# Kernel optimization log

Hardware: AMD Instinct MI355X
Metric: run time of the kernel (lower is better)

The kernel has to match this reference:

```python
import jax, jax.numpy as jnp
import numpy as np

B, T, C_IN, HID, WIN = 16384, 20, 256, 256, 3


def tb_mask(T=20, win=3):
    # Faithful replica of TemporalCrossAttent.TB (including its quirky indexing).
    m = np.zeros((T, T), dtype=np.float32)
    for i in range(T):
        if i - win < 0:
            m[i, :win] = 1
        elif i + win >= T:
            m[i, T - win:] = 1
        else:
            m[i - win // 2, i - win // 2:i + win // 2] = 1
    return jnp.asarray(np.where(m == 1, 0.0, -1e22).astype(np.float32))


def setup_inputs() -> dict:
    key = jax.random.key(0)
    k1, k2, k3, k4, k5 = jax.random.split(key, 5)
    scale = 0.05  # xavier-ish init scale for 256x256
    return {
        "feat1": jax.random.normal(k1, (B, T, C_IN), dtype=jnp.float32),
        "feat2": jax.random.normal(k2, (B, T, C_IN), dtype=jnp.float32),
        "Wq": jax.random.normal(k3, (HID, C_IN), dtype=jnp.float32) * scale,
        "Wk": jax.random.normal(k4, (HID, C_IN), dtype=jnp.float32) * scale,
        "Wv": jax.random.normal(k5, (HID, C_IN), dtype=jnp.float32) * scale,
    }


def reference(feat1, feat2, Wq, Wk, Wv):
    # Conv1d(kernel_size=1, bias=False) == pointwise linear over channels.
    mask = tb_mask(T, WIN)  # [T, T] static banded additive mask
    q = jnp.einsum('btc,hc->bth', feat1, Wq)  # [B,T,HID]
    k = jnp.einsum('btc,hc->bth', feat2, Wk)
    v = jnp.einsum('btc,hc->bth', feat2, Wv)
    sim = jnp.einsum('bth,bsh->bts', q, k) / jnp.sqrt(jnp.float32(HID))
    attn = jax.nn.softmax(sim + mask, axis=-1)  # [B,T,T]
    # dropout layers act as identity in eval mode
    return jnp.einsum('bts,bsh->bth', attn, v)  # [B,T,HID]
```

## Files before the change

### kernel.cpp

```cpp
#include <hip/hip_runtime.h>
#include <stdint.h>

#define NBATCH 16384
#define TT     20
#define CC     256
#define FP     260
#define FB     520
#define LDK    264
#define TP     40
#define NT     256

typedef __bf16 bf16x8 __attribute__((ext_vector_type(8)));
typedef float  f32x4  __attribute__((ext_vector_type(4)));

#define GLL16(g, l) __builtin_amdgcn_global_load_lds( \
    (const __attribute__((address_space(1))) uint32_t*)(g), \
    (__attribute__((address_space(3))) uint32_t*)(l), 16, 0, 0)

#define BAR_VM()   do { asm volatile("s_waitcnt vmcnt(0) lgkmcnt(0)" ::: "memory"); \
                        __builtin_amdgcn_s_barrier(); } while (0)
#define BAR_LGKM() do { asm volatile("s_waitcnt lgkmcnt(0)" ::: "memory"); \
                        __builtin_amdgcn_s_barrier(); } while (0)

__constant__ int8_t c_CNT[TT] = {3,3,4,2,2,2,2,2,2,2,2,2,2,2,2,2,0,3,3,3};
__constant__ int8_t c_OFF[TT] = {0,3,6,10,12,14,16,18,20,22,24,26,28,30,32,34,0,36,39,42};
__constant__ int8_t c_PT[45]  = {0,0,0,1,1,1,2,2,2,2,3,3,4,4,5,5,6,6,7,7,8,8,9,9,
                                 10,10,11,11,12,12,13,13,14,14,15,15,17,17,17,18,18,18,19,19,19};
__constant__ int8_t c_PS[45]  = {0,1,2,0,1,2,0,1,2,3,3,4,4,5,5,6,6,7,7,8,8,9,9,10,
                                 10,11,11,12,12,13,13,14,14,15,15,16,17,18,19,17,18,19,17,18,19};

__device__ __forceinline__ uint16_t f2bf(float f) {
    __bf16 b = (__bf16)f;
    return __builtin_bit_cast(uint16_t, b);
}
__device__ __forceinline__ uint32_t pk2(float a, float b) {
    return (uint32_t)f2bf(a) | ((uint32_t)f2bf(b) << 16);
}
__device__ __forceinline__ float bflo(uint32_t u) { return __builtin_bit_cast(float, u << 16); }
__device__ __forceinline__ float bfhi(uint32_t u) { return __builtin_bit_cast(float, u & 0xffff0000u); }

__global__ void prep1_kernel(const float* __restrict__ Wq, const float* __restrict__ Wk,
                             const float* __restrict__ Wv, uint16_t* __restrict__ mqkT,
                             uint16_t* __restrict__ wvb) {
    const int n = blockIdx.x;
    const int k = threadIdx.x;
    float acc = 0.f;
    for (int h = 0; h < CC; ++h)
        acc = fmaf(Wk[h * CC + n], Wq[h * CC + k], acc);
    mqkT[n * CC + k] = f2bf(acc * 0.0625f);
    wvb[n * CC + k]  = f2bf(Wv[n * CC + k]);
}

__global__ void prep2_kernel(const uint16_t* __restrict__ mqkT, const uint16_t* __restrict__ wvb,
                             uint16_t* __restrict__ BqS, uint16_t* __restrict__ BvS) {
    const int bid = blockIdx.x;
    const int m  = bid >> 5;
    const int w  = (bid >> 3) & 3;
    const int kk = bid & 7;
    const int ct   = threadIdx.x >> 6;
    const int lane = threadIdx.x & 63;
    const uint16_t* src = m ? wvb : mqkT;
    uint16_t*       dst = m ? BvS : BqS;
    const int n   = w * 64 + ct * 16 + (lane & 15);
    const int col = kk * 32 + ((lane >> 4) << 3);
    uint4 v = *(const uint4*)(src + n * CC + col);
    *(uint4*)(dst + ((size_t)((w * 32 + kk * 4 + ct) * 64 + lane) << 3)) = v;
}

__device__ __forceinline__ bf16x8 ldb(const uint16_t* __restrict__ s, int r, int u) {
    return __builtin_bit_cast(bf16x8, *(const uint4*)(s + r * FB + (u << 3)));
}

__global__ __launch_bounds__(NT, 3)
void attn_main(const float* __restrict__ f1g, const float* __restrict__ f2g,
               const uint16_t* __restrict__ BqS, const uint16_t* __restrict__ BvS,
               float* __restrict__ outg) {
    __shared__ char smem[53632];
    float*    sF1f  = (float*)smem;
    float*    sF2f  = (float*)(smem + 20800);
    uint16_t* attnL = (uint16_t*)(smem + 41600);
    float*    s_simE = (float*)(smem + 42880);
    uint16_t* sT    = (uint16_t*)(smem + 43072);
    uint16_t* sFb1 = (uint16_t*)sF1f;
    uint16_t* sFb2 = (uint16_t*)sF2f;
    uint16_t* sVT  = (uint16_t*)smem;

    const int tid  = threadIdx.x;
    const int lane = tid & 63;
    const int w    = tid >> 6;
    const int l15  = lane & 15;
    const int q    = lane >> 4;
    const size_t base = (size_t)blockIdx.x * TT * CC;
    const float* f1 = f1g + base;
    const float* f2 = f2g + base;

#pragma unroll
    for (int j = 0; j < 5; ++j) {
        int r = w * 5 + j;
        GLL16(f1 + r * 256 + (lane << 2), sF1f + r * FP);
        GLL16(f2 + r * 256 + (lane << 2), sF2f + r * FP);
    }
    {
        uint32_t* aL = (uint32_t*)attnL;
#pragma unroll
        for (int rep = 0; rep < 2; ++rep) {
            int s = tid + (rep << 8);
            if (s < 320)
                aL[s] = ((s >> 4) == 16 && (s & 15) < 10) ? 0x3F803F80u : 0u;
        }
    }
    BAR_VM();

#pragma unroll
    for (int j = 0; j < 5; ++j) {
        int r = w * 5 + j;
        float4 v1 = *(const float4*)(sF1f + r * FP + (lane << 2));
        float4 v2 = *(const float4*)(sF2f + r * FP + (lane << 2));
        uint2 u1; u1.x = pk2(v1.x, v1.y); u1.y = pk2(v1.z, v1.w);
        uint2 u2; u2.x = pk2(v2.x, v2.y); u2.y = pk2(v2.z, v2.w);
        *(uint2*)(sFb1 + r * FB + (lane << 2)) = u1;
        *(uint2*)(sFb2 + r * FB + (lane << 2)) = u2;
    }
    BAR_LGKM();

    const uint16_t* bq = BqS + ((size_t)w << 14);
    const uint16_t* bv = BvS + ((size_t)w << 14);
    const int rB0 = l15;
    const int rB1 = (16 + l15 < TT) ? 16 + l15 : TT - 1;

    {
        f32x4 acc[4][2];
#pragma unroll
        for (int mt = 0; mt < 4; ++mt)
#pragma unroll
            for (int ct = 0; ct < 2; ++ct)
                acc[mt][ct] = f32x4{0.f, 0.f, 0.f, 0.f};
        __builtin_amdgcn_s_setprio(1);
#pragma unroll
        for (int kk = 0; kk < 8; ++kk) {
            const int u = (kk << 2) + q;
            bf16x8 b0 = ldb(sFb1, rB0, u);
            bf16x8 b1 = ldb(sFb1, rB1, u);
#pragma unroll
            for (int mt = 0; mt < 4; ++mt) {
                bf16x8 am = __builtin_bit_cast(bf16x8,
                    *(const uint4*)(bq + (((kk << 2) + mt) * 64 + lane) * 8));
                acc[mt][0] = __builtin_amdgcn_mfma_f32_16x16x32_bf16(am, b0, acc[mt][0], 0, 0, 0);
                acc[mt][1] = __builtin_amdgcn_mfma_f32_16x16x32_bf16(am, b1, acc[mt][1], 0, 0, 0);
            }
        }
        __builtin_amdgcn_s_setprio(0);
#pragma unroll
        for (int mt = 0; mt < 4; ++mt)
#pragma unroll
            for (int ct = 0; ct < 2; ++ct) {
                int t = ct * 16 + l15;
                if (t < TT) {
                    int h0 = (w << 6) + mt * 16 + (q << 2);
                    uint2 u2;
                    u2.x = pk2(acc[mt][ct][0], acc[mt][ct][1]);
                    u2.y = pk2(acc[mt][ct][2], acc[mt][ct][3]);
                    *(uint2*)&sT[t * LDK + h0] = u2;
                }
            }
    }
    BAR_LGKM();

    if (tid < 180) {
        int d = tid >> 2;
        int p = tid & 3;
        int t = c_PT[d], s = c_PS[d];
        const uint16_t* ap = sT + t * LDK + (p << 3);
        const uint16_t* bp = sFb2 + s * FB + (p << 3);
        float da = 0.f;
#pragma unroll
        for (int c = 0; c < 256; c += 32) {
            uint4 ua = *(const uint4*)(ap + c);
            uint4 ub = *(const uint4*)(bp + c);
            da = fmaf(bflo(ua.x), bflo(ub.x), da);
            da = fmaf(bfhi(ua.x), bfhi(ub.x), da);
            da = fmaf(bflo(ua.y), bflo(ub.y), da);
            da = fmaf(bfhi(ua.y), bfhi(ub.y), da);
            da = fmaf(bflo(ua.z), bflo(ub.z), da);
            da = fmaf(bfhi(ua.z), bfhi(ub.z), da);
            da = fmaf(bflo(ua.w), bflo(ub.w), da);
            da = fmaf(bfhi(ua.w), bfhi(ub.w), da);
        }
        da += __shfl_xor(da, 1);
        da += __shfl_xor(da, 2);
        if (p == 0) {
            float e = __expf(da);
            attnL[t * 32 + s] = f2bf(e);
            s_simE[d] = e;
        }
    }
    {
        f32x4 av[2][4];
#pragma unroll
        for (int rt = 0; rt < 2; ++rt)
#pragma unroll
            for (int ct = 0; ct < 4; ++ct)
                av[rt][ct] = f32x4{0.f, 0.f, 0.f, 0.f};
        __builtin_amdgcn_s_setprio(1);
#pragma unroll
        for (int kk = 0; kk < 8; ++kk) {
            const int u = (kk << 2) + q;
            bf16x8 a0 = ldb(sFb2, rB0, u);
            bf16x8 a1 = ldb(sFb2, rB1, u);
#pragma unroll
            for (int ct = 0; ct < 4; ++ct) {
                bf16x8 bm = __builtin_bit_cast(bf16x8,
                    *(const uint4*)(bv + (((kk << 2) + ct) * 64 + lane) * 8));
                av[0][ct] = __builtin_amdgcn_mfma_f32_16x16x32_bf16(a0, bm, av[0][ct], 0, 0, 0);
                av[1][ct] = __builtin_amdgcn_mfma_f32_16x16x32_bf16(a1, bm, av[1][ct], 0, 0, 0);
            }
        }
        __builtin_amdgcn_s_setprio(0);
#pragma unroll
        for (int ct = 0; ct < 4; ++ct) {
            int h = (w << 6) + ct * 16 + l15;
            {
                uint2 u2;
                u2.x = pk2(av[0][ct][0], av[0][ct][1]);
                u2.y = pk2(av[0][ct][2], av[0][ct][3]);
                *(uint2*)&sVT[h * TP + (q << 2)] = u2;
            }
            {
                uint2 u2;
                if (q == 0) {
                    u2.x = pk2(av[1][ct][0], av[1][ct][1]);
                    u2.y = pk2(av[1][ct][2], av[1][ct][3]);
                } else { u2.x = 0u; u2.y = 0u; }
                *(uint2*)&sVT[h * TP + 16 + (q << 2)] = u2;
            }
        }
    }
    BAR_LGKM();

    {
        bf16x8 pa0 = __builtin_bit_cast(bf16x8, *(const uint4*)&attnL[l15 * 32 + (q << 3)]);
        bf16x8 pa1 = __builtin_bit_cast(bf16x8, *(const uint4*)&attnL[(16 + l15) * 32 + (q << 3)]);
        const f32x4 z = f32x4{0.f, 0.f, 0.f, 0.f};
        f32x4 o[2][4];
        __builtin_amdgcn_s_setprio(1);
#pragma unroll
        for (int ct = 0; ct < 4; ++ct) {
            bf16x8 pb = __builtin_bit_cast(bf16x8,
                *(const uint4*)&sVT[((w << 6) + ct * 16 + l15) * TP + (q << 3)]);
            o[0][ct] = __builtin_amdgcn_mfma_f32_16x16x32_bf16(pa0, pb, z, 0, 0, 0);
            o[1][ct] = __builtin_amdgcn_mfma_f32_16x16x32_bf16(pa1, pb, z, 0, 0, 0);
        }
        __builtin_amdgcn_s_setprio(0);
#pragma unroll
        for (int rt = 0; rt < 2; ++rt)
#pragma unroll
            for (int j = 0; j < 4; ++j) {
                int t = rt * 16 + (q << 2) + j;
                if (t < TT) {
                    int cnt = c_CNT[t], off = c_OFF[t];
                    float rs = (cnt == 0) ? 20.0f : s_simE[off];
#pragma unroll
                    for (int jj = 1; jj < 4; ++jj)
                        if (jj < cnt) rs += s_simE[off + jj];
                    float iv = __builtin_amdgcn_rcpf(rs);
                    float* op = outg + base + (size_t)t * CC + (w << 6) + l15;
#pragma unroll
                    for (int ct = 0; ct < 4; ++ct)
                        op[ct * 16] = o[rt][ct][j] * iv;
                }
            }
    }
}

extern "C" void kernel_launch(void* const* d_in, const int* in_sizes, int n_in,
                              void* d_out, int out_size, void* d_ws, size_t ws_size,
                              hipStream_t stream) {
    const float* feat1 = (const float*)d_in[0];
    const float* feat2 = (const float*)d_in[1];
    const float* Wq    = (const float*)d_in[2];
    const float* Wk    = (const float*)d_in[3];
    const float* Wv    = (const float*)d_in[4];
    uint16_t* mqkT = (uint16_t*)d_ws;
    uint16_t* wvb  = mqkT + CC * CC;
    uint16_t* BqS  = wvb  + CC * CC;
    uint16_t* BvS  = BqS  + CC * CC;

    prep1_kernel<<<CC, CC, 0, stream>>>(Wq, Wk, Wv, mqkT, wvb);
    prep2_kernel<<<64, NT, 0, stream>>>(mqkT, wvb, BqS, BvS);
    attn_main<<<NBATCH, NT, 0, stream>>>(feat1, feat2, BqS, BvS, (float*)d_out);
}
```

Measured before the change: 384.1 us.

## Make attention blocks persistent over 32 batches with register-prefetched double-buffered inputs

Each workgroup now handles 32 batch elements in a loop instead of one. While it computes the current element, it loads the next element's feat1/feat2 into registers and converts them to bf16 into an alternate LDS buffer, replacing the global_load_lds path with fp32 staging. This is meant to hide global load latency and amortize launch and setup overhead. In exchange, the grid shrinks to 512 blocks (a few per CU), register pressure rises, and launch bounds drop to 2 waves-per-EU occupancy, which may reduce latency hiding.

```diff
diff --git a/kernel.cpp b/kernel.cpp
--- a/kernel.cpp
+++ b/kernel.cpp
@@ -4,21 +4,14 @@
 #define NBATCH 16384
 #define TT     20
 #define CC     256
-#define FP     260
-#define FB     520
-#define LDK    264
-#define TP     40
+#define LDB    264
+#define TP     32
 #define NT     256
+#define BPB    32
 
 typedef __bf16 bf16x8 __attribute__((ext_vector_type(8)));
 typedef float  f32x4  __attribute__((ext_vector_type(4)));
 
-#define GLL16(g, l) __builtin_amdgcn_global_load_lds( \
-    (const __attribute__((address_space(1))) uint32_t*)(g), \
-    (__attribute__((address_space(3))) uint32_t*)(l), 16, 0, 0)
-
-#define BAR_VM()   do { asm volatile("s_waitcnt vmcnt(0) lgkmcnt(0)" ::: "memory"); \
-                        __builtin_amdgcn_s_barrier(); } while (0)
 #define BAR_LGKM() do { asm volatile("s_waitcnt lgkmcnt(0)" ::: "memory"); \
                         __builtin_amdgcn_s_barrier(); } while (0)
 
@@ -68,60 +61,24 @@
 }
 
 __device__ __forceinline__ bf16x8 ldb(const uint16_t* __restrict__ s, int r, int u) {
-    return __builtin_bit_cast(bf16x8, *(const uint4*)(s + r * FB + (u << 3)));
-}
-
-__global__ __launch_bounds__(NT, 3)
+    return __builtin_bit_cast(bf16x8, *(const uint4*)(s + r * LDB + (u << 3)));
+}
+
+__global__ __launch_bounds__(NT, 2)
 void attn_main(const float* __restrict__ f1g, const float* __restrict__ f2g,
                const uint16_t* __restrict__ BqS, const uint16_t* __restrict__ BvS,
                float* __restrict__ outg) {
-    __shared__ char smem[53632];
-    float*    sF1f  = (float*)smem;
-    float*    sF2f  = (float*)(smem + 20800);
-    uint16_t* attnL = (uint16_t*)(smem + 41600);
-    float*    s_simE = (float*)(smem + 42880);
-    uint16_t* sT    = (uint16_t*)(smem + 43072);
-    uint16_t* sFb1 = (uint16_t*)sF1f;
-    uint16_t* sFb2 = (uint16_t*)sF2f;
-    uint16_t* sVT  = (uint16_t*)smem;
+    __shared__ uint16_t smem[30048];
+    uint16_t* sVT    = smem + 21120;
+    uint16_t* attnL  = smem + 29312;
+    float*    s_simE = (float*)(smem + 29952);
 
     const int tid  = threadIdx.x;
     const int lane = tid & 63;
     const int w    = tid >> 6;
     const int l15  = lane & 15;
     const int q    = lane >> 4;
-    const size_t base = (size_t)blockIdx.x * TT * CC;
-    const float* f1 = f1g + base;
-    const float* f2 = f2g + base;
-
-#pragma unroll
-    for (int j = 0; j < 5; ++j) {
-        int r = w * 5 + j;
-        GLL16(f1 + r * 256 + (lane << 2), sF1f + r * FP);
-        GLL16(f2 + r * 256 + (lane << 2), sF2f + r * FP);
-    }
-    {
-        uint32_t* aL = (uint32_t*)attnL;
-#pragma unroll
-        for (int rep = 0; rep < 2; ++rep) {
-            int s = tid + (rep << 8);
-            if (s < 320)
-                aL[s] = ((s >> 4) == 16 && (s & 15) < 10) ? 0x3F803F80u : 0u;
-        }
-    }
-    BAR_VM();
-
-#pragma unroll
-    for (int j = 0; j < 5; ++j) {
-        int r = w * 5 + j;
-        float4 v1 = *(const float4*)(sF1f + r * FP + (lane << 2));
-        float4 v2 = *(const float4*)(sF2f + r * FP + (lane << 2));
-        uint2 u1; u1.x = pk2(v1.x, v1.y); u1.y = pk2(v1.z, v1.w);
-        uint2 u2; u2.x = pk2(v2.x, v2.y); u2.y = pk2(v2.z, v2.w);
-        *(uint2*)(sFb1 + r * FB + (lane << 2)) = u1;
-        *(uint2*)(sFb2 + r * FB + (lane << 2)) = u2;
-    }
-    BAR_LGKM();
+    const size_t bbase = (size_t)blockIdx.x * BPB * TT * CC;
 
     const uint16_t* bq = BqS + ((size_t)w << 14);
     const uint16_t* bv = BvS + ((size_t)w << 14);
@@ -129,146 +86,209 @@
     const int rB1 = (16 + l15 < TT) ? 16 + l15 : TT - 1;
 
     {
-        f32x4 acc[4][2];
-#pragma unroll
-        for (int mt = 0; mt < 4; ++mt)
-#pragma unroll
-            for (int ct = 0; ct < 2; ++ct)
-                acc[mt][ct] = f32x4{0.f, 0.f, 0.f, 0.f};
-        __builtin_amdgcn_s_setprio(1);
-#pragma unroll
-        for (int kk = 0; kk < 8; ++kk) {
-            const int u = (kk << 2) + q;
-            bf16x8 b0 = ldb(sFb1, rB0, u);
-            bf16x8 b1 = ldb(sFb1, rB1, u);
-#pragma unroll
-            for (int mt = 0; mt < 4; ++mt) {
-                bf16x8 am = __builtin_bit_cast(bf16x8,
-                    *(const uint4*)(bq + (((kk << 2) + mt) * 64 + lane) * 8));
-                acc[mt][0] = __builtin_amdgcn_mfma_f32_16x16x32_bf16(am, b0, acc[mt][0], 0, 0, 0);
-                acc[mt][1] = __builtin_amdgcn_mfma_f32_16x16x32_bf16(am, b1, acc[mt][1], 0, 0, 0);
-            }
-        }
-        __builtin_amdgcn_s_setprio(0);
-#pragma unroll
-        for (int mt = 0; mt < 4; ++mt)
-#pragma unroll
-            for (int ct = 0; ct < 2; ++ct) {
-                int t = ct * 16 + l15;
-                if (t < TT) {
-                    int h0 = (w << 6) + mt * 16 + (q << 2);
-                    uint2 u2;
-                    u2.x = pk2(acc[mt][ct][0], acc[mt][ct][1]);
-                    u2.y = pk2(acc[mt][ct][2], acc[mt][ct][3]);
-                    *(uint2*)&sT[t * LDK + h0] = u2;
-                }
-            }
+        const float* f1 = f1g + bbase;
+        const float* f2 = f2g + bbase;
+        float4 va[5], vb[5];
+#pragma unroll
+        for (int j = 0; j < 5; ++j) {
+            int s = tid + (j << 8);
+            va[j] = *(const float4*)(f1 + (s << 2));
+            vb[j] = *(const float4*)(f2 + (s << 2));
+        }
+        {
+            uint32_t* aL = (uint32_t*)attnL;
+#pragma unroll
+            for (int rep = 0; rep < 2; ++rep) {
+                int s = tid + (rep << 8);
+                if (s < 320)
+                    aL[s] = ((s >> 4) == 16 && (s & 15) < 10) ? 0x3F803F80u : 0u;
+            }
+        }
+#pragma unroll
+        for (int j = 0; j < 5; ++j) {
+            int s  = tid + (j << 8);
+            int r  = s >> 6;
+            int c4 = (s & 63) << 2;
+            uint2 u1; u1.x = pk2(va[j].x, va[j].y); u1.y = pk2(va[j].z, va[j].w);
+            uint2 u2; u2.x = pk2(vb[j].x, vb[j].y); u2.y = pk2(vb[j].z, vb[j].w);
+            *(uint2*)&smem[r * LDB + c4] = u1;
+            *(uint2*)&smem[5280 + r * LDB + c4] = u2;
+        }
     }
     BAR_LGKM();
 
-    if (tid < 180) {
-        int d = tid >> 2;
-        int p = tid & 3;
-        int t = c_PT[d], s = c_PS[d];
-        const uint16_t* ap = sT + t * LDK + (p << 3);
-        const uint16_t* bp = sFb2 + s * FB + (p << 3);
-        float da = 0.f;
-#pragma unroll
-        for (int c = 0; c < 256; c += 32) {
-            uint4 ua = *(const uint4*)(ap + c);
-            uint4 ub = *(const uint4*)(bp + c);
-            da = fmaf(bflo(ua.x), bflo(ub.x), da);
-            da = fmaf(bfhi(ua.x), bfhi(ub.x), da);
-            da = fmaf(bflo(ua.y), bflo(ub.y), da);
-            da = fmaf(bfhi(ua.y), bfhi(ub.y), da);
-            da = fmaf(bflo(ua.z), bflo(ub.z), da);
-            da = fmaf(bfhi(ua.z), bfhi(ub.z), da);
-            da = fmaf(bflo(ua.w), bflo(ub.w), da);
-            da = fmaf(bfhi(ua.w), bfhi(ub.w), da);
-        }
-        da += __shfl_xor(da, 1);
-        da += __shfl_xor(da, 2);
-        if (p == 0) {
-            float e = __expf(da);
-            attnL[t * 32 + s] = f2bf(e);
-            s_simE[d] = e;
-        }
-    }
-    {
-        f32x4 av[2][4];
-#pragma unroll
-        for (int rt = 0; rt < 2; ++rt)
-#pragma unroll
-            for (int ct = 0; ct < 4; ++ct)
-                av[rt][ct] = f32x4{0.f, 0.f, 0.f, 0.f};
-        __builtin_amdgcn_s_setprio(1);
-#pragma unroll
-        for (int kk = 0; kk < 8; ++kk) {
-            const int u = (kk << 2) + q;
-            bf16x8 a0 = ldb(sFb2, rB0, u);
-            bf16x8 a1 = ldb(sFb2, rB1, u);
+    for (int i = 0; i < BPB; ++i) {
+        const int curOf = (i & 1) ? 10560 : 0;
+        const int nxtOf = (i & 1) ? 0 : 10560;
+        const bool hasNext = (i + 1 < BPB);
+        const uint16_t* f1b = smem + curOf;
+        const uint16_t* f2b = smem + curOf + 5280;
+        uint16_t* sT = smem + nxtOf;
+        uint16_t* w2 = smem + nxtOf + 5280;
+
+        float4 pa[5], pb[5];
+        if (hasNext) {
+            const float* f1n = f1g + bbase + (size_t)(i + 1) * TT * CC;
+            const float* f2n = f2g + bbase + (size_t)(i + 1) * TT * CC;
+#pragma unroll
+            for (int j = 0; j < 5; ++j) {
+                int s = tid + (j << 8);
+                pa[j] = *(const float4*)(f1n + (s << 2));
+                pb[j] = *(const float4*)(f2n + (s << 2));
+            }
+            __builtin_amdgcn_sched_barrier(0);
+        }
+
+        {
+            f32x4 acc[4][2];
+#pragma unroll
+            for (int mt = 0; mt < 4; ++mt)
+#pragma unroll
+                for (int ct = 0; ct < 2; ++ct)
+                    acc[mt][ct] = f32x4{0.f, 0.f, 0.f, 0.f};
+#pragma unroll
+            for (int kk = 0; kk < 8; ++kk) {
+                const int u = (kk << 2) + q;
+                bf16x8 b0 = ldb(f1b, rB0, u);
+                bf16x8 b1 = ldb(f1b, rB1, u);
+#pragma unroll
+                for (int mt = 0; mt < 4; ++mt) {
+                    bf16x8 am = __builtin_bit_cast(bf16x8,
+                        *(const uint4*)(bq + (((kk << 2) + mt) * 64 + lane) * 8));
+                    acc[mt][0] = __builtin_amdgcn_mfma_f32_16x16x32_bf16(am, b0, acc[mt][0], 0, 0, 0);
+                    acc[mt][1] = __builtin_amdgcn_mfma_f32_16x16x32_bf16(am, b1, acc[mt][1], 0, 0, 0);
+                }
+            }
+#pragma unroll
+            for (int mt = 0; mt < 4; ++mt)
+#pragma unroll
+                for (int ct = 0; ct < 2; ++ct) {
+                    int t = ct * 16 + l15;
+                    if (t < TT) {
+                        int h0 = (w << 6) + mt * 16 + (q << 2);
+                        uint2 u2;
+                        u2.x = pk2(acc[mt][ct][0], acc[mt][ct][1]);
+                        u2.y = pk2(acc[mt][ct][2], acc[mt][ct][3]);
+                        *(uint2*)&sT[t * LDB + h0] = u2;
+                    }
+                }
+        }
+        BAR_LGKM();
+
+        if (tid < 180) {
+            int d = tid >> 2;
+            int p = tid & 3;
+            int t = c_PT[d], s = c_PS[d];
+            const uint16_t* ap = sT  + t * LDB + (p << 3);
+            const uint16_t* bp = f2b + s * LDB + (p << 3);
+            float da = 0.f;
+#pragma unroll
+            for (int c = 0; c < 256; c += 32) {
+                uint4 ua = *(const uint4*)(ap + c);
+                uint4 ub = *(const uint4*)(bp + c);
+                da = fmaf(bflo(ua.x), bflo(ub.x), da);
+                da = fmaf(bfhi(ua.x), bfhi(ub.x), da);
+                da = fmaf(bflo(ua.y), bflo(ub.y), da);
+                da = fmaf(bfhi(ua.y), bfhi(ub.y), da);
+                da = fmaf(bflo(ua.z), bflo(ub.z), da);
+                da = fmaf(bfhi(ua.z), bfhi(ub.z), da);
+                da = fmaf(bflo(ua.w), bflo(ub.w), da);
+                da = fmaf(bfhi(ua.w), bfhi(ub.w), da);
+            }
+            da += __shfl_xor(da, 1);
+            da += __shfl_xor(da, 2);
+            if (p == 0) {
+                float e = __expf(da);
+                attnL[t * 32 + s] = f2bf(e);
+                s_simE[d] = e;
+            }
+        }
+        {
+            f32x4 av[2][4];
+#pragma unroll
+            for (int rt = 0; rt < 2; ++rt)
+#pragma unroll
+                for (int ct = 0; ct < 4; ++ct)
+                    av[rt][ct] = f32x4{0.f, 0.f, 0.f, 0.f};
+#pragma unroll
+            for (int kk = 0; kk < 8; ++kk) {
+                const int u = (kk << 2) + q;
+                bf16x8 a0 = ldb(f2b, rB0, u);
+                bf16x8 a1 = ldb(f2b, rB1, u);
+#pragma unroll
+                for (int ct = 0; ct < 4; ++ct) {
+                    bf16x8 bm = __builtin_bit_cast(bf16x8,
+                        *(const uint4*)(bv + (((kk << 2) + ct) * 64 + lane) * 8));
+                    av[0][ct] = __builtin_amdgcn_mfma_f32_16x16x32_bf16(a0, bm, av[0][ct], 0, 0, 0);
+                    av[1][ct] = __builtin_amdgcn_mfma_f32_16x16x32_bf16(a1, bm, av[1][ct], 0, 0, 0);
+                }
+            }
 #pragma unroll
             for (int ct = 0; ct < 4; ++ct) {
-                bf16x8 bm = __builtin_bit_cast(bf16x8,
-                    *(const uint4*)(bv + (((kk << 2) + ct) * 64 + lane) * 8));
-                av[0][ct] = __builtin_amdgcn_mfma_f32_16x16x32_bf16(a0, bm, av[0][ct], 0, 0, 0);
-                av[1][ct] = __builtin_amdgcn_mfma_f32_16x16x32_bf16(a1, bm, av[1][ct], 0, 0, 0);
-            }
-        }
-        __builtin_amdgcn_s_setprio(0);
-#pragma unroll
-        for (int ct = 0; ct < 4; ++ct) {
-            int h = (w << 6) + ct * 16 + l15;
-            {
-                uint2 u2;
-                u2.x = pk2(av[0][ct][0], av[0][ct][1]);
-                u2.y = pk2(av[0][ct][2], av[0][ct][3]);
-                *(uint2*)&sVT[h * TP + (q << 2)] = u2;
-            }
-            {
-                uint2 u2;
-                if (q == 0) {
-                    u2.x = pk2(av[1][ct][0], av[1][ct][1]);
-                    u2.y = pk2(av[1][ct][2], av[1][ct][3]);
-                } else { u2.x = 0u; u2.y = 0u; }
-                *(uint2*)&sVT[h * TP + 16 + (q << 2)] = u2;
-            }
-        }
-    }
-    BAR_LGKM();
-
-    {
-        bf16x8 pa0 = __builtin_bit_cast(bf16x8, *(const uint4*)&attnL[l15 * 32 + (q << 3)]);
-        bf16x8 pa1 = __builtin_bit_cast(bf16x8, *(const uint4*)&attnL[(16 + l15) * 32 + (q << 3)]);
-        const f32x4 z = f32x4{0.f, 0.f, 0.f, 0.f};
-        f32x4 o[2][4];
-        __builtin_amdgcn_s_setprio(1);
-#pragma unroll
-        for (int ct = 0; ct < 4; ++ct) {
-            bf16x8 pb = __builtin_bit_cast(bf16x8,
-                *(const uint4*)&sVT[((w << 6) + ct * 16 + l15) * TP + (q << 3)]);
-            o[0][ct] = __builtin_amdgcn_mfma_f32_16x16x32_bf16(pa0, pb, z, 0, 0, 0);
-            o[1][ct] = __builtin_amdgcn_mfma_f32_16x16x32_bf16(pa1, pb, z, 0, 0, 0);
-        }
-        __builtin_amdgcn_s_setprio(0);
-#pragma unroll
-        for (int rt = 0; rt < 2; ++rt)
-#pragma unroll
-            for (int j = 0; j < 4; ++j) {
-                int t = rt * 16 + (q << 2) + j;
-                if (t < TT) {
-                    int cnt = c_CNT[t], off = c_OFF[t];
-                    float rs = (cnt == 0) ? 20.0f : s_simE[off];
-#pragma unroll
-                    for (int jj = 1; jj < 4; ++jj)
-                        if (jj < cnt) rs += s_simE[off + jj];
-                    float iv = __builtin_amdgcn_rcpf(rs);
-                    float* op = outg + base + (size_t)t * CC + (w << 6) + l15;
-#pragma unroll
-                    for (int ct = 0; ct < 4; ++ct)
-                        op[ct * 16] = o[rt][ct][j] * iv;
-                }
-            }
+                int h = (w << 6) + ct * 16 + l15;
+                {
+                    uint2 u2;
+                    u2.x = pk2(av[0][ct][0], av[0][ct][1]);
+                    u2.y = pk2(av[0][ct][2], av[0][ct][3]);
+                    *(uint2*)&sVT[h * TP + (q << 2)] = u2;
+                }
+                {
+                    uint2 u2;
+                    if (q == 0) {
+                        u2.x = pk2(av[1][ct][0], av[1][ct][1]);
+                        u2.y = pk2(av[1][ct][2], av[1][ct][3]);
+                    } else { u2.x = 0u; u2.y = 0u; }
+                    *(uint2*)&sVT[h * TP + 16 + (q << 2)] = u2;
+                }
+            }
+        }
+        BAR_LGKM();
+
+        {
+            bf16x8 pa0 = __builtin_bit_cast(bf16x8, *(const uint4*)&attnL[l15 * 32 + (q << 3)]);
+            bf16x8 pa1 = __builtin_bit_cast(bf16x8, *(const uint4*)&attnL[(16 + l15) * 32 + (q << 3)]);
+            const f32x4 z = f32x4{0.f, 0.f, 0.f, 0.f};
+            f32x4 o[2][4];
+#pragma unroll
+            for (int ct = 0; ct < 4; ++ct) {
+                bf16x8 pbv = __builtin_bit_cast(bf16x8,
+                    *(const uint4*)&sVT[((w << 6) + ct * 16 + l15) * TP + (q << 3)]);
+                o[0][ct] = __builtin_amdgcn_mfma_f32_16x16x32_bf16(pa0, pbv, z, 0, 0, 0);
+                o[1][ct] = __builtin_amdgcn_mfma_f32_16x16x32_bf16(pa1, pbv, z, 0, 0, 0);
+            }
+            const size_t ob = bbase + (size_t)i * TT * CC;
+#pragma unroll
+            for (int rt = 0; rt < 2; ++rt)
+#pragma unroll
+                for (int j = 0; j < 4; ++j) {
+                    int t = rt * 16 + (q << 2) + j;
+                    if (t < TT) {
+                        int cnt = c_CNT[t], off = c_OFF[t];
+                        float rs = (cnt == 0) ? 20.0f : s_simE[off];
+#pragma unroll
+                        for (int jj = 1; jj < 4; ++jj)
+                            if (jj < cnt) rs += s_simE[off + jj];
+                        float iv = __builtin_amdgcn_rcpf(rs);
+                        float* op = outg + ob + (size_t)t * CC + (w << 6) + l15;
+#pragma unroll
+                        for (int ct = 0; ct < 4; ++ct)
+                            op[ct * 16] = o[rt][ct][j] * iv;
+                    }
+                }
+        }
+        if (hasNext) {
+#pragma unroll
+            for (int j = 0; j < 5; ++j) {
+                int s  = tid + (j << 8);
+                int r  = s >> 6;
+                int c4 = (s & 63) << 2;
+                uint2 u1; u1.x = pk2(pa[j].x, pa[j].y); u1.y = pk2(pa[j].z, pa[j].w);
+                uint2 u2; u2.x = pk2(pb[j].x, pb[j].y); u2.y = pk2(pb[j].z, pb[j].w);
+                *(uint2*)&sT[r * LDB + c4] = u1;
+                *(uint2*)&w2[r * LDB + c4] = u2;
+            }
+        }
+        BAR_LGKM();
     }
 }
 
@@ -287,5 +307,5 @@
 
     prep1_kernel<<<CC, CC, 0, stream>>>(Wq, Wk, Wv, mqkT, wvb);
     prep2_kernel<<<64, NT, 0, stream>>>(mqkT, wvb, BqS, BvS);
-    attn_main<<<NBATCH, NT, 0, stream>>>(feat1, feat2, BqS, BvS, (float*)d_out);
-}
+    attn_main<<<NBATCH / BPB, NT, 0, stream>>>(feat1, feat2, BqS, BvS, (float*)d_out);
+}
```

Result: slower. 820.8 us (+113.7%).
